# Kernel optimization log

Hardware: AMD Instinct MI355X
Metric: run time of the kernel (lower is better)

Reference implementation:

```python
import jax, jax.numpy as jnp
import numpy as np

N_NODES = 50000


def gcn_layer(x, src, dst, ew, W, b, n_nodes):
    # PyG GCNConv: add self-loops (weight 1), symmetric deg^-1/2 normalization,
    # linear transform, scatter-add aggregation at destination, then bias.
    loop = jnp.arange(n_nodes, dtype=src.dtype)
    s = jnp.concatenate([src, loop])
    d = jnp.concatenate([dst, loop])
    w = jnp.concatenate([ew, jnp.ones((n_nodes,), dtype=ew.dtype)])
    deg = jax.ops.segment_sum(w, d, num_segments=n_nodes)  # [N]
    dinv = jnp.where(deg > 0, jax.lax.rsqrt(jnp.where(deg > 0, deg, 1.0)), 0.0)
    norm = dinv[s] * w * dinv[d]  # [E+N]
    h = x @ W  # [N, out]
    msg = h[s] * norm[:, None]  # gather + scale, [E+N, out]
    out = jax.ops.segment_sum(msg, d, num_segments=n_nodes)  # scatter-add
    return out + b


def setup_inputs() -> dict:
    key = jax.random.key(0)
    k1, k2, k3, k4, k5, k6, k7 = jax.random.split(key, 7)
    N, E, C_IN, C_OUT = N_NODES, 600000, 128, 128
    x = jax.random.normal(k1, (N, C_IN), dtype=jnp.float32)
    edge_index = jax.random.randint(k2, (2, E), 0, N, dtype=jnp.int64)
    edge_weight = jax.random.uniform(k3, (E,), dtype=jnp.float32)
    # Glorot-style init like PyG's Linear default
    s1 = 1.0 / np.sqrt(C_IN)
    s2 = 1.0 / np.sqrt(C_OUT)
    W1 = jax.random.uniform(k4, (C_IN, C_OUT), jnp.float32, -s1, s1)
    b1 = jnp.zeros((C_OUT,), dtype=jnp.float32)
    W2 = jax.random.uniform(k5, (C_OUT, C_OUT), jnp.float32, -s2, s2)
    b2 = jnp.zeros((C_OUT,), dtype=jnp.float32)
    return {"x": x, "edge_index": edge_index, "edge_weight": edge_weight,
            "W1": W1, "b1": b1, "W2": W2, "b2": b2}


def reference(x, edge_index, edge_weight, W1, b1, W2, b2):
    src, dst = edge_index[0], edge_index[1]
    h = jax.nn.relu(gcn_layer(x, src, dst, edge_weight, W1, b1, N_NODES))
    return jax.nn.relu(gcn_layer(h, src, dst, edge_weight, W2, b2, N_NODES))
```

## Files before the change

### kernel.cpp

```cpp
#include <hip/hip_runtime.h>
#include <math.h>

#define CH   128
#define CH4  32
#define TPB  256
#define SCANB 1024
#define WIMG 16384
#define NREP 4

typedef __attribute__((ext_vector_type(8))) short short8;
typedef __attribute__((ext_vector_type(4))) float floatx4;

static __device__ __forceinline__ unsigned short f2bf(float f) {
    unsigned u = __float_as_uint(f);
    return (unsigned short)((u + 0x7fffu + ((u >> 16) & 1u)) >> 16);
}
static __device__ __forceinline__ float bf2f(unsigned short s) {
    return __uint_as_float(((unsigned)s) << 16);
}
static __device__ __forceinline__ float4 bf4_to_f4(ushort4 u) {
    return make_float4(bf2f(u.x), bf2f(u.y), bf2f(u.z), bf2f(u.w));
}

__global__ void k_prep(const float* __restrict__ W1, const float* __restrict__ W2,
                       short* __restrict__ Wsplit) {
    int i = blockIdx.x * blockDim.x + threadIdx.x;
    if (i >= 2 * CH * CH) return;
    int layer = i >> 14;
    int idx   = i & 16383;
    int k = idx >> 7, c = idx & 127;
    float w = (layer ? W2 : W1)[k * CH + c];
    unsigned short hi = f2bf(w);
    unsigned short lo = f2bf(w - bf2f(hi));
    int colh = c >> 6, nn = c & 63;
    int kt = k >> 5, q = (k & 31) >> 3, j = k & 7;
    int ns = nn >> 4, ln = q * 16 + (nn & 15);
    size_t base = (size_t)(layer * 2 + colh) * WIMG;
    size_t off  = ((size_t)(kt * 4 + ns) * 64 + ln) * 8 + j;
    Wsplit[base + off]        = (short)hi;
    Wsplit[base + 8192 + off] = (short)lo;
}

#define STAGE_W(sW, Wfrag, tid)                                    \
    {                                                              \
        const float4* gsrc = (const float4*)(Wfrag);               \
        float4* ldst = (float4*)(sW);                              \
        _Pragma("unroll")                                          \
        for (int i = 0; i < 8; ++i)                                \
            ldst[i * TPB + (tid)] = gsrc[i * TPB + (tid)];         \
    }

static __device__ __forceinline__ void gemm_body_f32(
        const float* __restrict__ X, const short* __restrict__ Wfrag,
        unsigned short* __restrict__ H, int n, int tile, int colh, int tid) {
    __shared__ __align__(16) short sW[2][4][4][64][8];
    STAGE_W(sW, Wfrag, tid);
    __syncthreads();

    const int lane = tid & 63;
    const int wv   = tid >> 6;
    const int q    = lane >> 4;
    const int m    = lane & 15;
    const int row0 = tile * 64 + wv * 16;
    if (row0 >= n) return;

    int rrow = row0 + m;
    if (rrow > n - 1) rrow = n - 1;

    const float4* xr = (const float4*)(X + (size_t)rrow * CH);
    float4 xa[4][2];
    #pragma unroll
    for (int kt = 0; kt < 4; ++kt) {
        xa[kt][0] = xr[kt * 8 + q * 2 + 0];
        xa[kt][1] = xr[kt * 8 + q * 2 + 1];
    }

    floatx4 acc[4];
    #pragma unroll
    for (int ns = 0; ns < 4; ++ns) acc[ns] = (floatx4){0.f, 0.f, 0.f, 0.f};

    #pragma unroll
    for (int kt = 0; kt < 4; ++kt) {
        float xf[8] = { xa[kt][0].x, xa[kt][0].y, xa[kt][0].z, xa[kt][0].w,
                        xa[kt][1].x, xa[kt][1].y, xa[kt][1].z, xa[kt][1].w };
        short8 ah, al;
        #pragma unroll
        for (int j = 0; j < 8; ++j) {
            float v = xf[j];
            unsigned short h = f2bf(v);
            ah[j] = (short)h;
            al[j] = (short)f2bf(v - bf2f(h));
        }
        #pragma unroll
        for (int ns = 0; ns < 4; ++ns) {
            short8 bh = *(const short8*)&sW[0][kt][ns][lane][0];
            short8 bl = *(const short8*)&sW[1][kt][ns][lane][0];
            acc[ns] = __builtin_amdgcn_mfma_f32_16x16x32_bf16(ah, bh, acc[ns], 0, 0, 0);
            acc[ns] = __builtin_amdgcn_mfma_f32_16x16x32_bf16(al, bh, acc[ns], 0, 0, 0);
            acc[ns] = __builtin_amdgcn_mfma_f32_16x16x32_bf16(ah, bl, acc[ns], 0, 0, 0);
        }
    }

    #pragma unroll
    for (int ns = 0; ns < 4; ++ns) {
        #pragma unroll
        for (int reg = 0; reg < 4; ++reg) {
            int r = row0 + q * 4 + reg;
            if (r < n)
                H[(size_t)r * CH + colh * 64 + ns * 16 + m] = f2bf(acc[ns][reg]);
        }
    }
}

static __device__ __forceinline__ void gemm_body_bf(
        const unsigned short* __restrict__ X, const short* __restrict__ Wfrag,
        unsigned short* __restrict__ H, int n, int tile, int colh, int tid) {
    __shared__ __align__(16) short sW[2][4][4][64][8];
    STAGE_W(sW, Wfrag, tid);
    __syncthreads();

    const int lane = tid & 63;
    const int wv   = tid >> 6;
    const int q    = lane >> 4;
    const int m    = lane & 15;
    const int row0 = tile * 64 + wv * 16;
    if (row0 >= n) return;

    int rrow = row0 + m;
    if (rrow > n - 1) rrow = n - 1;

    const ushort4* xr = (const ushort4*)(X + (size_t)rrow * CH);
    short8 a[4];
    #pragma unroll
    for (int kt = 0; kt < 4; ++kt) {
        ushort4 u0 = xr[kt * 8 + q * 2 + 0];
        ushort4 u1 = xr[kt * 8 + q * 2 + 1];
        a[kt][0] = (short)u0.x; a[kt][1] = (short)u0.y;
        a[kt][2] = (short)u0.z; a[kt][3] = (short)u0.w;
        a[kt][4] = (short)u1.x; a[kt][5] = (short)u1.y;
        a[kt][6] = (short)u1.z; a[kt][7] = (short)u1.w;
    }

    floatx4 acc[4];
    #pragma unroll
    for (int ns = 0; ns < 4; ++ns) acc[ns] = (floatx4){0.f, 0.f, 0.f, 0.f};

    #pragma unroll
    for (int kt = 0; kt < 4; ++kt) {
        #pragma unroll
        for (int ns = 0; ns < 4; ++ns) {
            short8 bh = *(const short8*)&sW[0][kt][ns][lane][0];
            short8 bl = *(const short8*)&sW[1][kt][ns][lane][0];
            acc[ns] = __builtin_amdgcn_mfma_f32_16x16x32_bf16(a[kt], bh, acc[ns], 0, 0, 0);
            acc[ns] = __builtin_amdgcn_mfma_f32_16x16x32_bf16(a[kt], bl, acc[ns], 0, 0, 0);
        }
    }

    #pragma unroll
    for (int ns = 0; ns < 4; ++ns) {
        #pragma unroll
        for (int reg = 0; reg < 4; ++reg) {
            int r = row0 + q * 4 + reg;
            if (r < n)
                H[(size_t)r * CH + colh * 64 + ns * 16 + m] = f2bf(acc[ns][reg]);
        }
    }
}

__global__ __launch_bounds__(TPB, 4)
void k_gemm_rank(const float* __restrict__ X, const short* __restrict__ Wsplit,
                 unsigned short* __restrict__ H, int n,
                 const int* __restrict__ dst, int* __restrict__ counts_rep,
                 int* __restrict__ rank, int E, int nbE, int Np) {
    int bx = blockIdx.x;
    if (bx < nbE) {
        int e = bx * TPB + threadIdx.x;
        if (e < E) {
            int d = dst[e];
            if ((unsigned)d < (unsigned)n) {
                int rep = e & (NREP - 1);
                rank[e] = atomicAdd(&counts_rep[rep * Np + d], 1);
            }
        }
    } else {
        bx -= nbE;
        int colh = bx & 1;
        gemm_body_f32(X, Wsplit + (size_t)colh * WIMG, H, n, bx >> 1, colh,
                      threadIdx.x);
    }
}

__global__ __launch_bounds__(TPB, 4)
void k_gemm_bf(const unsigned short* __restrict__ X, const short* __restrict__ Wsplit,
               unsigned short* __restrict__ H, int n) {
    int colh = (int)blockIdx.x & 1;
    gemm_body_bf(X, Wsplit + (size_t)colh * WIMG, H, n,
                 (int)blockIdx.x >> 1, colh, threadIdx.x);
}

__global__ __launch_bounds__(SCANB)
void k_scan1(const int* __restrict__ counts_rep, int Np,
             int* __restrict__ counts_tot, int4* __restrict__ repoff,
             int* __restrict__ row_start, int* __restrict__ partials, int n) {
    __shared__ int s[SCANB];
    int gid = blockIdx.x * SCANB + threadIdx.x;
    int c0 = 0, c1 = 0, c2 = 0, c3 = 0;
    if (gid < n) {
        c0 = counts_rep[gid];
        c1 = counts_rep[Np + gid];
        c2 = counts_rep[2 * Np + gid];
        c3 = counts_rep[3 * Np + gid];
    }
    int v = c0 + c1 + c2 + c3;
    s[threadIdx.x] = v;
    __syncthreads();
    for (int off = 1; off < SCANB; off <<= 1) {
        int t = (threadIdx.x >= off) ? s[threadIdx.x - off] : 0;
        __syncthreads();
        s[threadIdx.x] += t;
        __syncthreads();
    }
    if (gid < n) {
        row_start[gid]  = s[threadIdx.x] - v;
        counts_tot[gid] = v;
        repoff[gid]     = make_int4(0, c0, c0 + c1, c0 + c1 + c2);
    }
    if (threadIdx.x == SCANB - 1) partials[blockIdx.x] = s[SCANB - 1];
}

__global__ __launch_bounds__(SCANB)
void k_scan3(int* __restrict__ row_start, const int* __restrict__ partials, int n) {
    __shared__ int sbase;
    if (threadIdx.x < 64) {
        int v = (threadIdx.x < blockIdx.x) ? partials[threadIdx.x] : 0;
        #pragma unroll
        for (int off = 32; off; off >>= 1) v += __shfl_down(v, off, 64);
        if (threadIdx.x == 0) sbase = v;
    }
    __syncthreads();
    int gid = blockIdx.x * SCANB + threadIdx.x;
    if (gid < n) row_start[gid] += sbase;
}

__global__ void k_fill(const int* __restrict__ src, const int* __restrict__ dst,
                       const float* __restrict__ ew, const int* __restrict__ row_start,
                       const int4* __restrict__ repoff, const int* __restrict__ rank,
                       int2* __restrict__ edges, int E, int n) {
    int e = blockIdx.x * blockDim.x + threadIdx.x;
    if (e >= E) return;
    int s = src[e], d = dst[e];
    if ((unsigned)s >= (unsigned)n || (unsigned)d >= (unsigned)n) return;
    int rep = e & (NREP - 1);
    int4 ro = repoff[d];
    int roa[4] = {ro.x, ro.y, ro.z, ro.w};
    edges[row_start[d] + roa[rep] + rank[e]] = make_int2(s, __float_as_int(ew[e]));
}

__global__ void k_deg(const int* __restrict__ row_start, const int* __restrict__ counts,
                      const int2* __restrict__ edges, float* __restrict__ dinv, int n) {
    int i = blockIdx.x * blockDim.x + threadIdx.x;
    if (i >= n) return;
    int j = row_start[i], end = j + counts[i];
    float sum = 1.0f;
    for (; j < end; ++j) sum += __int_as_float(edges[j].y);
    dinv[i] = rsqrtf(sum);
}

template<int RELU_OUT, int FIXUP, int OUT_BF16>
__global__ __launch_bounds__(TPB)
void k_aggregate(const unsigned short* __restrict__ h, const int* __restrict__ row_start,
                 const int* __restrict__ counts, int2* __restrict__ edges,
                 const float* __restrict__ dinv, const float* __restrict__ bias,
                 void* __restrict__ out, int n) {
    int t = blockIdx.x * blockDim.x + threadIdx.x;
    int node = t >> 5;
    if (node >= n) return;
    int tx = t & 31;

    const ushort4* h4 = (const ushort4*)h;
    float di = dinv[node];
    float4 b  = ((const float4*)bias)[tx];
    float4 hv = bf4_to_f4(h4[(size_t)node * CH4 + tx]);
    float4 acc = make_float4(0.f, 0.f, 0.f, 0.f);

    int j   = row_start[node];
    int end = j + counts[node];

    for (; j + 8 <= end; j += 8) {
        int2 e[8];
        #pragma unroll
        for (int i = 0; i < 8; ++i) e[i] = edges[j + i];
        ushort4 g[8];
        #pragma unroll
        for (int i = 0; i < 8; ++i) g[i] = h4[(size_t)e[i].x * CH4 + tx];
        float w[8];
        #pragma unroll
        for (int i = 0; i < 8; ++i) {
            w[i] = __int_as_float(e[i].y);
            if (FIXUP) w[i] *= dinv[e[i].x];
        }
        if (FIXUP && tx == 0) {
            #pragma unroll
            for (int i = 0; i < 8; ++i) edges[j + i].y = __float_as_int(w[i]);
        }
        #pragma unroll
        for (int i = 0; i < 8; ++i) {
            float4 gf = bf4_to_f4(g[i]);
            acc.x += gf.x * w[i]; acc.y += gf.y * w[i];
            acc.z += gf.z * w[i]; acc.w += gf.w * w[i];
        }
    }
    if (j + 4 <= end) {
        int2 e[4];
        #pragma unroll
        for (int i = 0; i < 4; ++i) e[i] = edges[j + i];
        ushort4 g[4];
        #pragma unroll
        for (int i = 0; i < 4; ++i) g[i] = h4[(size_t)e[i].x * CH4 + tx];
        float w[4];
        #pragma unroll
        for (int i = 0; i < 4; ++i) {
            w[i] = __int_as_float(e[i].y);
            if (FIXUP) w[i] *= dinv[e[i].x];
        }
        if (FIXUP && tx == 0) {
            #pragma unroll
            for (int i = 0; i < 4; ++i) edges[j + i].y = __float_as_int(w[i]);
        }
        #pragma unroll
        for (int i = 0; i < 4; ++i) {
            float4 gf = bf4_to_f4(g[i]);
            acc.x += gf.x * w[i]; acc.y += gf.y * w[i];
            acc.z += gf.z * w[i]; acc.w += gf.w * w[i];
        }
        j += 4;
    }
    for (; j < end; ++j) {
        int2 e0 = edges[j];
        float w0 = __int_as_float(e0.y);
        if (FIXUP) w0 *= dinv[e0.x];
        if (FIXUP && tx == 0) edges[j].y = __float_as_int(w0);
        float4 gf = bf4_to_f4(h4[(size_t)e0.x * CH4 + tx]);
        acc.x += gf.x * w0; acc.y += gf.y * w0;
        acc.z += gf.z * w0; acc.w += gf.w * w0;
    }

    float sc = di * di;
    float4 o = make_float4(hv.x * sc + b.x + di * acc.x,
                           hv.y * sc + b.y + di * acc.y,
                           hv.z * sc + b.z + di * acc.z,
                           hv.w * sc + b.w + di * acc.w);
    if (RELU_OUT) {
        o.x = fmaxf(o.x, 0.f); o.y = fmaxf(o.y, 0.f);
        o.z = fmaxf(o.z, 0.f); o.w = fmaxf(o.w, 0.f);
    }
    if (OUT_BF16) {
        ushort4 u = make_ushort4(f2bf(o.x), f2bf(o.y), f2bf(o.z), f2bf(o.w));
        ((ushort4*)out)[(size_t)node * CH4 + tx] = u;
    } else {
        ((float4*)out)[(size_t)node * CH4 + tx] = o;
    }
}

extern "C" void kernel_launch(void* const* d_in, const int* in_sizes, int n_in,
                              void* d_out, int out_size, void* d_ws, size_t ws_size,
                              hipStream_t stream) {
    const float* x  = (const float*)d_in[0];
    const int*   ei = (const int*)d_in[1];
    const float* ew = (const float*)d_in[2];
    const float* W1 = (const float*)d_in[3];
    const float* b1 = (const float*)d_in[4];
    const float* W2 = (const float*)d_in[5];
    const float* b2 = (const float*)d_in[6];
    float* out = (float*)d_out;

    const int N = in_sizes[0] / CH;
    const int E = in_sizes[2];
    const int* src = ei;
    const int* dst = ei + E;

    size_t Np = ((size_t)N + 255) & ~(size_t)255;
    size_t Ep = ((size_t)E + 63) & ~(size_t)63;
    float* ws          = (float*)d_ws;
    float* dinv        = ws;
    unsigned short* h  = (unsigned short*)(dinv + Np);
    unsigned short* o1 = h + (size_t)N * CH;
    int*  counts_rep   = (int*)(o1 + (size_t)N * CH);
    int*  counts_tot   = counts_rep + NREP * Np;
    int*  row_start    = counts_tot + Np;
    int4* repoff       = (int4*)(row_start + Np);
    int*  rank         = (int*)(repoff + Np);
    int*  partials     = rank + Ep;
    int2* edges        = (int2*)(partials + 64);
    short* Wsplit      = (short*)(edges + E);

    const int nbN    = (N + TPB - 1) / TPB;
    const int nbE    = (E + TPB - 1) / TPB;
    const int nbAgg  = (int)(((size_t)N * 32 + TPB - 1) / TPB);
    const int nbScan = (N + SCANB - 1) / SCANB;
    const int nbGemm2 = 2 * ((N + 63) / 64);
    const int nbPrep  = (2 * CH * CH + TPB - 1) / TPB;

    hipMemsetAsync(counts_rep, 0, (size_t)NREP * Np * sizeof(int), stream);
    k_prep     <<<nbPrep, TPB, 0, stream>>>(W1, W2, Wsplit);

    k_gemm_rank<<<nbE + nbGemm2, TPB, 0, stream>>>(x, Wsplit, h, N, dst,
                                                   counts_rep, rank, E, nbE, (int)Np);
    k_scan1    <<<nbScan, SCANB, 0, stream>>>(counts_rep, (int)Np, counts_tot,
                                              repoff, row_start, partials, N);
    k_scan3    <<<nbScan, SCANB, 0, stream>>>(row_start, partials, N);
    k_fill     <<<nbE, TPB, 0, stream>>>(src, dst, ew, row_start, repoff, rank,
                                         edges, E, N);
    k_deg      <<<nbN, TPB, 0, stream>>>(row_start, counts_tot, edges, dinv, N);

    k_aggregate<1,1,1><<<nbAgg, TPB, 0, stream>>>(h, row_start, counts_tot, edges,
                                                  dinv, b1, o1, N);
    k_gemm_bf         <<<nbGemm2, TPB, 0, stream>>>(o1, Wsplit + 2 * WIMG, h, N);
    k_aggregate<1,0,0><<<nbAgg, TPB, 0, stream>>>(h, row_start, counts_tot, edges,
                                                  dinv, b2, out, N);
}
```

Before: 224.4 us.

## Fold degree computation into rank pass and merge scan kernels via last-block fixup

```diff
diff --git a/kernel.cpp b/kernel.cpp
--- a/kernel.cpp
+++ b/kernel.cpp
@@ -129,17 +129,10 @@
     int rrow = row0 + m;
     if (rrow > n - 1) rrow = n - 1;
 
-    const ushort4* xr = (const ushort4*)(X + (size_t)rrow * CH);
+    const short8* xr8 = (const short8*)(X + (size_t)rrow * CH);
     short8 a[4];
     #pragma unroll
-    for (int kt = 0; kt < 4; ++kt) {
-        ushort4 u0 = xr[kt * 8 + q * 2 + 0];
-        ushort4 u1 = xr[kt * 8 + q * 2 + 1];
-        a[kt][0] = (short)u0.x; a[kt][1] = (short)u0.y;
-        a[kt][2] = (short)u0.z; a[kt][3] = (short)u0.w;
-        a[kt][4] = (short)u1.x; a[kt][5] = (short)u1.y;
-        a[kt][6] = (short)u1.z; a[kt][7] = (short)u1.w;
-    }
+    for (int kt = 0; kt < 4; ++kt) a[kt] = xr8[kt * 4 + q];
 
     floatx4 acc[4];
     #pragma unroll
@@ -170,7 +163,8 @@
 __global__ __launch_bounds__(TPB, 4)
 void k_gemm_rank(const float* __restrict__ X, const short* __restrict__ Wsplit,
                  unsigned short* __restrict__ H, int n,
-                 const int* __restrict__ dst, int* __restrict__ counts_rep,
+                 const int* __restrict__ dst, const float* __restrict__ ew,
+                 int* __restrict__ counts_rep, float* __restrict__ deg_rep,
                  int* __restrict__ rank, int E, int nbE, int Np) {
     int bx = blockIdx.x;
     if (bx < nbE) {
@@ -180,6 +174,7 @@
             if ((unsigned)d < (unsigned)n) {
                 int rep = e & (NREP - 1);
                 rank[e] = atomicAdd(&counts_rep[rep * Np + d], 1);
+                unsafeAtomicAdd(&deg_rep[rep * Np + d], ew[e]);
             }
         }
     } else {
@@ -199,10 +194,13 @@
 }
 
 __global__ __launch_bounds__(SCANB)
-void k_scan1(const int* __restrict__ counts_rep, int Np,
-             int* __restrict__ counts_tot, int4* __restrict__ repoff,
-             int* __restrict__ row_start, int* __restrict__ partials, int n) {
+void k_scan1(const int* __restrict__ counts_rep, const float* __restrict__ deg_rep,
+             int Np, int* __restrict__ counts_tot, int4* __restrict__ repoff,
+             int* __restrict__ row_start, float* __restrict__ dinv,
+             int* __restrict__ partials, int* __restrict__ pp_s,
+             int* __restrict__ done, int nb, int n) {
     __shared__ int s[SCANB];
+    __shared__ int slast;
     int gid = blockIdx.x * SCANB + threadIdx.x;
     int c0 = 0, c1 = 0, c2 = 0, c3 = 0;
     if (gid < n) {
@@ -210,6 +208,9 @@
         c1 = counts_rep[Np + gid];
         c2 = counts_rep[2 * Np + gid];
         c3 = counts_rep[3 * Np + gid];
+        float dsum = 1.0f + deg_rep[gid] + deg_rep[Np + gid]
+                   + deg_rep[2 * Np + gid] + deg_rep[3 * Np + gid];
+        dinv[gid] = rsqrtf(dsum);
     }
     int v = c0 + c1 + c2 + c3;
     s[threadIdx.x] = v;
@@ -225,27 +226,30 @@
         counts_tot[gid] = v;
         repoff[gid]     = make_int4(0, c0, c0 + c1, c0 + c1 + c2);
     }
-    if (threadIdx.x == SCANB - 1) partials[blockIdx.x] = s[SCANB - 1];
-}
-
-__global__ __launch_bounds__(SCANB)
-void k_scan3(int* __restrict__ row_start, const int* __restrict__ partials, int n) {
-    __shared__ int sbase;
-    if (threadIdx.x < 64) {
-        int v = (threadIdx.x < blockIdx.x) ? partials[threadIdx.x] : 0;
-        #pragma unroll
-        for (int off = 32; off; off >>= 1) v += __shfl_down(v, off, 64);
-        if (threadIdx.x == 0) sbase = v;
+    if (threadIdx.x == SCANB - 1) {
+        partials[blockIdx.x] = s[SCANB - 1];
+        __threadfence();
+        int old = atomicAdd(done, 1);
+        slast = (old == nb - 1);
     }
     __syncthreads();
-    int gid = blockIdx.x * SCANB + threadIdx.x;
-    if (gid < n) row_start[gid] += sbase;
+    if (slast && threadIdx.x < 64) {
+        int pv = (threadIdx.x < nb) ? atomicAdd(&partials[threadIdx.x], 0) : 0;
+        int inc = pv;
+        #pragma unroll
+        for (int off = 1; off < 64; off <<= 1) {
+            int t = __shfl_up(inc, off, 64);
+            if ((threadIdx.x & 63) >= off) inc += t;
+        }
+        if (threadIdx.x < nb) pp_s[threadIdx.x] = inc - pv;
+    }
 }
 
 __global__ void k_fill(const int* __restrict__ src, const int* __restrict__ dst,
                        const float* __restrict__ ew, const int* __restrict__ row_start,
-                       const int4* __restrict__ repoff, const int* __restrict__ rank,
-                       int2* __restrict__ edges, int E, int n) {
+                       const int* __restrict__ pp_s, const int4* __restrict__ repoff,
+                       const int* __restrict__ rank, int2* __restrict__ edges,
+                       int E, int n) {
     int e = blockIdx.x * blockDim.x + threadIdx.x;
     if (e >= E) return;
     int s = src[e], d = dst[e];
@@ -253,25 +257,16 @@
     int rep = e & (NREP - 1);
     int4 ro = repoff[d];
     int roa[4] = {ro.x, ro.y, ro.z, ro.w};
-    edges[row_start[d] + roa[rep] + rank[e]] = make_int2(s, __float_as_int(ew[e]));
-}
-
-__global__ void k_deg(const int* __restrict__ row_start, const int* __restrict__ counts,
-                      const int2* __restrict__ edges, float* __restrict__ dinv, int n) {
-    int i = blockIdx.x * blockDim.x + threadIdx.x;
-    if (i >= n) return;
-    int j = row_start[i], end = j + counts[i];
-    float sum = 1.0f;
-    for (; j < end; ++j) sum += __int_as_float(edges[j].y);
-    dinv[i] = rsqrtf(sum);
+    int base = row_start[d] + pp_s[d >> 10];
+    edges[base + roa[rep] + rank[e]] = make_int2(s, __float_as_int(ew[e]));
 }
 
 template<int RELU_OUT, int FIXUP, int OUT_BF16>
 __global__ __launch_bounds__(TPB)
 void k_aggregate(const unsigned short* __restrict__ h, const int* __restrict__ row_start,
-                 const int* __restrict__ counts, int2* __restrict__ edges,
-                 const float* __restrict__ dinv, const float* __restrict__ bias,
-                 void* __restrict__ out, int n) {
+                 const int* __restrict__ pp_s, const int* __restrict__ counts,
+                 int2* __restrict__ edges, const float* __restrict__ dinv,
+                 const float* __restrict__ bias, void* __restrict__ out, int n) {
     int t = blockIdx.x * blockDim.x + threadIdx.x;
     int node = t >> 5;
     if (node >= n) return;
@@ -283,7 +278,7 @@
     float4 hv = bf4_to_f4(h4[(size_t)node * CH4 + tx]);
     float4 acc = make_float4(0.f, 0.f, 0.f, 0.f);
 
-    int j   = row_start[node];
+    int j   = row_start[node] + pp_s[node >> 10];
     int end = j + counts[node];
 
     for (; j + 8 <= end; j += 8) {
@@ -385,37 +380,41 @@
     float* dinv        = ws;
     unsigned short* h  = (unsigned short*)(dinv + Np);
     unsigned short* o1 = h + (size_t)N * CH;
-    int*  counts_rep   = (int*)(o1 + (size_t)N * CH);
-    int*  counts_tot   = counts_rep + NREP * Np;
+    int*   counts_rep  = (int*)(o1 + (size_t)N * CH);
+    float* deg_rep     = (float*)(counts_rep + NREP * Np);
+    int*   done        = (int*)(deg_rep + NREP * Np);
+    size_t zero_bytes  = (size_t)(2 * NREP) * Np * 4 + 256;
+    int*  counts_tot   = done + 64;
     int*  row_start    = counts_tot + Np;
     int4* repoff       = (int4*)(row_start + Np);
     int*  rank         = (int*)(repoff + Np);
     int*  partials     = rank + Ep;
-    int2* edges        = (int2*)(partials + 64);
+    int*  pp_s         = partials + 64;
+    int2* edges        = (int2*)(pp_s + 64);
     short* Wsplit      = (short*)(edges + E);
 
-    const int nbN    = (N + TPB - 1) / TPB;
     const int nbE    = (E + TPB - 1) / TPB;
     const int nbAgg  = (int)(((size_t)N * 32 + TPB - 1) / TPB);
     const int nbScan = (N + SCANB - 1) / SCANB;
     const int nbGemm2 = 2 * ((N + 63) / 64);
     const int nbPrep  = (2 * CH * CH + TPB - 1) / TPB;
 
-    hipMemsetAsync(counts_rep, 0, (size_t)NREP * Np * sizeof(int), stream);
+    hipMemsetAsync(counts_rep, 0, zero_bytes, stream);
     k_prep     <<<nbPrep, TPB, 0, stream>>>(W1, W2, Wsplit);
 
-    k_gemm_rank<<<nbE + nbGemm2, TPB, 0, stream>>>(x, Wsplit, h, N, dst,
-                                                   counts_rep, rank, E, nbE, (int)Np);
-    k_scan1    <<<nbScan, SCANB, 0, stream>>>(counts_rep, (int)Np, counts_tot,
-                                              repoff, row_start, partials, N);
-    k_scan3    <<<nbScan, SCANB, 0, stream>>>(row_start, partials, N);
-    k_fill     <<<nbE, TPB, 0, stream>>>(src, dst, ew, row_start, repoff, rank,
-                                         edges, E, N);
-    k_deg      <<<nbN, TPB, 0, stream>>>(row_start, counts_tot, edges, dinv, N);
-
-    k_aggregate<1,1,1><<<nbAgg, TPB, 0, stream>>>(h, row_start, counts_tot, edges,
-                                                  dinv, b1, o1, N);
+    k_gemm_rank<<<nbE + nbGemm2, TPB, 0, stream>>>(x, Wsplit, h, N, dst, ew,
+                                                   counts_rep, deg_rep, rank,
+                                                   E, nbE, (int)Np);
+    k_scan1    <<<nbScan, SCANB, 0, stream>>>(counts_rep, deg_rep, (int)Np,
+                                              counts_tot, repoff, row_start,
+                                              dinv, partials, pp_s, done,
+                                              nbScan, N);
+    k_fill     <<<nbE, TPB, 0, stream>>>(src, dst, ew, row_start, pp_s, repoff,
+                                         rank, edges, E, N);
+
+    k_aggregate<1,1,1><<<nbAgg, TPB, 0, stream>>>(h, row_start, pp_s, counts_tot,
+                                                  edges, dinv, b1, o1, N);
     k_gemm_bf         <<<nbGemm2, TPB, 0, stream>>>(o1, Wsplit + 2 * WIMG, h, N);
-    k_aggregate<1,0,0><<<nbAgg, TPB, 0, stream>>>(h, row_start, counts_tot, edges,
-                                                  dinv, b2, out, N);
-}
+    k_aggregate<1,0,0><<<nbAgg, TPB, 0, stream>>>(h, row_start, pp_s, counts_tot,
+                                                  edges, dinv, b2, out, N);
+}
```

Result: slower. 247.6 us (+10.3%).
